# Kernel tuning notes

Hardware: AMD Instinct MI355X
Metric: run time of the kernel (lower is better)

The kernel has to match this reference:

```python
import jax, jax.numpy as jnp
import numpy as np

DIM = 1024
HEADS = 16
HEAD_DIM = DIM // HEADS
HIDDEN = DIM * 4
EPS = 1e-6


def _layernorm(x, g, b):
    mu = jnp.mean(x, axis=-1, keepdims=True)
    var = jnp.mean(jnp.square(x - mu), axis=-1, keepdims=True)
    return (x - mu) * jax.lax.rsqrt(var + EPS) * g + b


def setup_inputs() -> dict:
    key = jax.random.key(0)
    ks = jax.random.split(key, 12)
    s = 0.02
    return {
        "x": jax.random.normal(ks[0], (16, 1024, DIM), dtype=jnp.float32),
        "ln1_g": jnp.ones((DIM,), jnp.float32),
        "ln1_b": jnp.zeros((DIM,), jnp.float32),
        "qkv_w": jax.random.normal(ks[1], (DIM, 3 * DIM), jnp.float32) * s,
        "qkv_b": jnp.zeros((3 * DIM,), jnp.float32),
        "proj_w": jax.random.normal(ks[2], (DIM, DIM), jnp.float32) * s,
        "proj_b": jnp.zeros((DIM,), jnp.float32),
        "ls1_g": jnp.ones((DIM,), jnp.float32),
        "ln2_g": jnp.ones((DIM,), jnp.float32),
        "ln2_b": jnp.zeros((DIM,), jnp.float32),
        "fc1_w": jax.random.normal(ks[3], (DIM, HIDDEN), jnp.float32) * s,
        "fc1_b": jnp.zeros((HIDDEN,), jnp.float32),
        "fc2_w": jax.random.normal(ks[4], (HIDDEN, DIM), jnp.float32) * s,
        "fc2_b": jnp.zeros((DIM,), jnp.float32),
        "ls2_g": jnp.ones((DIM,), jnp.float32),
    }


def reference(x, ln1_g, ln1_b, qkv_w, qkv_b, proj_w, proj_b, ls1_g,
              ln2_g, ln2_b, fc1_w, fc1_b, fc2_w, fc2_b, ls2_g):
    B, N, C = x.shape
    # --- attention branch (NOTE: original code omits 1/sqrt(d) scaling) ---
    h = _layernorm(x, ln1_g, ln1_b)
    qkv = (h @ qkv_w + qkv_b).reshape(B, N, 3, HEADS, HEAD_DIM)
    q, k, v = jnp.moveaxis(qkv, 2, 0)          # each [B, N, H, D]
    attn = jnp.einsum("bqhd,bkhd->bhqk", q, k)  # no scale, faithful to source
    attn = jax.nn.softmax(attn, axis=-1)
    out = jnp.einsum("bhqk,bkhd->bqhd", attn, v).reshape(B, N, C)
    x = x + (out @ proj_w + proj_b) * ls1_g
    # --- MLP branch ---
    h = _layernorm(x, ln2_g, ln2_b)
    h = jax.nn.gelu(h @ fc1_w + fc1_b, approximate=False)
    x = x + (h @ fc2_w + fc2_b) * ls2_g
    return x
```

## Files before the change

kernel.cpp:

```cpp
#include <hip/hip_runtime.h>
#include <hip/hip_bf16.h>
#include <math.h>

typedef __attribute__((ext_vector_type(8))) short short8;
typedef __attribute__((ext_vector_type(4))) float f32x4;

#define MFMA16(a,b,c) __builtin_amdgcn_mfma_f32_16x16x32_bf16((a),(b),(c),0,0,0)

__device__ __forceinline__ unsigned short f2bf(float f){
  unsigned int u = __builtin_bit_cast(unsigned int, f);
  u += 0x7fffu + ((u >> 16) & 1u);
  return (unsigned short)(u >> 16);
}

__device__ __forceinline__ void gload16(const void* g, void* lds){
  __builtin_amdgcn_global_load_lds(
      (const __attribute__((address_space(1))) unsigned int*)g,
      (__attribute__((address_space(3))) unsigned int*)lds, 16, 0, 0);
}

__global__ __launch_bounds__(256) void k_transpose_cast(const float* __restrict__ in,
    unsigned short* __restrict__ out, int K, int N)
{
  __shared__ unsigned short tile[32][33];
  const int tx = threadIdx.x, ty = threadIdx.y;
  const int n0 = blockIdx.x * 32, k0 = blockIdx.y * 32;
  #pragma unroll
  for (int i = 0; i < 4; i++) {
    int k = k0 + ty + i*8;
    tile[ty + i*8][tx] = f2bf(in[(size_t)k * N + n0 + tx]);
  }
  __syncthreads();
  #pragma unroll
  for (int i = 0; i < 4; i++) {
    int n = n0 + ty + i*8;
    out[(size_t)n * K + k0 + tx] = tile[tx][ty + i*8];
  }
}

__global__ __launch_bounds__(256) void k_layernorm(const float* __restrict__ x,
    const float* __restrict__ g, const float* __restrict__ b,
    unsigned short* __restrict__ out)
{
  const int row = blockIdx.x;
  const int t = threadIdx.x;
  const float4 v = ((const float4*)(x + (size_t)row * 1024))[t];
  float s  = v.x + v.y + v.z + v.w;
  float s2 = v.x*v.x + v.y*v.y + v.z*v.z + v.w*v.w;
  #pragma unroll
  for (int m = 1; m < 64; m <<= 1) {
    s  += __shfl_xor(s,  m);
    s2 += __shfl_xor(s2, m);
  }
  __shared__ float red[2][4];
  const int wid = t >> 6, lane = t & 63;
  if (lane == 0) { red[0][wid] = s; red[1][wid] = s2; }
  __syncthreads();
  s  = red[0][0] + red[0][1] + red[0][2] + red[0][3];
  s2 = red[1][0] + red[1][1] + red[1][2] + red[1][3];
  const float mu = s * (1.0f / 1024.0f);
  const float var = s2 * (1.0f / 1024.0f) - mu * mu;
  const float rstd = rsqrtf(var + 1e-6f);
  const float4 gv = ((const float4*)g)[t];
  const float4 bv = ((const float4*)b)[t];
  ushort4 o;
  o.x = f2bf((v.x - mu) * rstd * gv.x + bv.x);
  o.y = f2bf((v.y - mu) * rstd * gv.y + bv.y);
  o.z = f2bf((v.z - mu) * rstd * gv.z + bv.z);
  o.w = f2bf((v.w - mu) * rstd * gv.w + bv.w);
  ((ushort4*)(out + (size_t)row * 1024))[t] = o;
}

template<int EPI>
__global__ __launch_bounds__(256, 3) void k_gemm128(
    const unsigned short* __restrict__ A,
    const unsigned short* __restrict__ Bt,
    const float* __restrict__ bias,
    const float* __restrict__ resid,
    const float* __restrict__ lsg,
    void* __restrict__ outp,
    unsigned short* __restrict__ vtp,
    int M, int N, int K, int nbn)
{
  __shared__ __align__(16) unsigned short Asm[128 * 32];
  __shared__ __align__(16) unsigned short Bsm[128 * 32];

  const int bid = blockIdx.x;
  const int mrows = (gridDim.x >> 3) / nbn;
  const int xcd = bid & 7, l = bid >> 3;
  const int bm = xcd * mrows + (l % mrows);
  const int bn = l / mrows;

  const int t = threadIdx.x, lane = t & 63;
  const int wid = t >> 6, wm = wid >> 1, wn = wid & 1;
  const int fr = lane & 15, fg = lane >> 4;

  const int r0 = t >> 2;
  const int c0 = ((t & 3) ^ ((r0 >> 2) & 3)) * 8;
  const int r1 = (256 + t) >> 2;
  const int c1 = (((256 + t) & 3) ^ ((r1 >> 2) & 3)) * 8;
  const size_t a0 = ((size_t)bm * 128 + r0) * K + c0;
  const size_t a1 = ((size_t)bm * 128 + r1) * K + c1;
  const size_t b0 = ((size_t)bn * 128 + r0) * K + c0;
  const size_t b1 = ((size_t)bn * 128 + r1) * K + c1;

  f32x4 acc[4][4] = {};

  for (int kt = 0; kt < K; kt += 32) {
    __syncthreads();
    gload16(A  + a0 + kt, (char*)Asm + t * 16);
    gload16(A  + a1 + kt, (char*)Asm + 4096 + t * 16);
    gload16(Bt + b0 + kt, (char*)Bsm + t * 16);
    gload16(Bt + b1 + kt, (char*)Bsm + 4096 + t * 16);
    __syncthreads();
    short8 af[4], bfv[4];
    #pragma unroll
    for (int m = 0; m < 4; m++) {
      const int row = wm * 64 + m * 16 + fr;
      af[m] = *(const short8*)((const char*)Asm + row * 64
                               + ((fg ^ ((row >> 2) & 3)) * 16));
    }
    #pragma unroll
    for (int n = 0; n < 4; n++) {
      const int row = wn * 64 + n * 16 + fr;
      bfv[n] = *(const short8*)((const char*)Bsm + row * 64
                                + ((fg ^ ((row >> 2) & 3)) * 16));
    }
    #pragma unroll
    for (int m = 0; m < 4; m++)
      #pragma unroll
      for (int n = 0; n < 4; n++)
        acc[m][n] = MFMA16(af[m], bfv[n], acc[m][n]);
  }

  const int row0 = bm * 128 + wm * 64 + fg * 4;
  const int col0 = bn * 128 + wn * 64 + fr;
  #pragma unroll
  for (int n = 0; n < 4; n++) {
    const int col = col0 + n * 16;
    const float bcol = bias[col];
    float lscale = 0.f;
    if (EPI == 2) lscale = lsg[col];
    #pragma unroll
    for (int m = 0; m < 4; m++) {
      #pragma unroll
      for (int r = 0; r < 4; r++) {
        const int row = row0 + m * 16 + r;
        float v = acc[m][n][r] + bcol;
        if (EPI == 0) {
          if (bn < 16) {
            ((unsigned short*)outp)[(size_t)row * 2048 + col] = f2bf(v);
          } else {
            const int d = col - 2048, hh = d >> 6, dd = d & 63;
            const int bb = row >> 10, nn = row & 1023;
            vtp[(((size_t)bb * 16 + hh) * 64 + dd) * 1024 + nn] = f2bf(v);
          }
        } else if (EPI == 1) {
          const float u = v * (0.7978845608f + 0.0356774081f * v * v);
          v = v * __builtin_amdgcn_rcpf(1.0f + __expf(-2.0f * u));
          ((unsigned short*)outp)[(size_t)row * N + col] = f2bf(v);
        } else {
          ((float*)outp)[(size_t)row * N + col] =
              resid[(size_t)row * N + col] + v * lscale;
        }
      }
    }
  }
}

__global__ __launch_bounds__(512) void k_attn(const unsigned short* __restrict__ qk,
                                              const unsigned short* __restrict__ vT,
                                              unsigned short* __restrict__ out)
{
  const int qt = blockIdx.x;
  const int bh = blockIdx.y;
  const int b = bh >> 4, h = bh & 15;
  const int t = threadIdx.x, lane = t & 63, wid = t >> 6;
  const int fr = lane & 15, fg = lane >> 4;
  const int q0 = qt * 256 + wid * 32;

  __shared__ __align__(16) unsigned short Ksm[64 * 64];
  __shared__ __align__(16) unsigned short Vsm[64 * 64];
  __shared__ __align__(16) unsigned short plds[8][32][72];

  const size_t qbase = (size_t)b * 1024 * 2048 + (size_t)h * 64;
  const size_t kbase = qbase + 1024;
  const size_t vbase = (size_t)bh * 64 * 1024;

  short8 qf[2][2];
  #pragma unroll
  for (int m = 0; m < 2; m++)
    #pragma unroll
    for (int kh = 0; kh < 2; kh++)
      qf[m][kh] = *(const short8*)(qk + qbase + (size_t)(q0 + m*16 + fr) * 2048
                                   + kh*32 + fg*8);

  f32x4 oacc[2][4] = {};
  float mrow[2][4], lrow[2][4];
  #pragma unroll
  for (int m = 0; m < 2; m++)
    #pragma unroll
    for (int r = 0; r < 4; r++) { mrow[m][r] = -1e30f; lrow[m][r] = 0.f; }

  const int srow = t >> 3, sc = t & 7;
  const int scs = sc ^ (srow & 7);

  for (int kv0 = 0; kv0 < 1024; kv0 += 64) {
    __syncthreads();
    gload16(qk + kbase + (size_t)(kv0 + srow) * 2048 + scs*8, (char*)Ksm + t*16);
    gload16(vT + vbase + (size_t)srow * 1024 + kv0 + scs*8,   (char*)Vsm + t*16);
    __syncthreads();

    f32x4 sacc[2][4] = {};
    #pragma unroll
    for (int n = 0; n < 4; n++) {
      #pragma unroll
      for (int kh = 0; kh < 2; kh++) {
        const int krow = n*16 + fr;
        short8 kf = *(const short8*)&Ksm[krow*64 + (((kh*4 + fg) ^ (krow & 7)) * 8)];
        sacc[0][n] = MFMA16(qf[0][kh], kf, sacc[0][n]);
        sacc[1][n] = MFMA16(qf[1][kh], kf, sacc[1][n]);
      }
    }

    #pragma unroll
    for (int m = 0; m < 2; m++) {
      float pm[4];
      #pragma unroll
      for (int r = 0; r < 4; r++)
        pm[r] = fmaxf(fmaxf(sacc[m][0][r], sacc[m][1][r]),
                      fmaxf(sacc[m][2][r], sacc[m][3][r]));
      #pragma unroll
      for (int msk = 1; msk < 16; msk <<= 1)
        #pragma unroll
        for (int r = 0; r < 4; r++) pm[r] = fmaxf(pm[r], __shfl_xor(pm[r], msk));
      float corr[4];
      #pragma unroll
      for (int r = 0; r < 4; r++) {
        float mn = fmaxf(mrow[m][r], pm[r]);
        corr[r] = __expf(mrow[m][r] - mn);
        mrow[m][r] = mn;
      }
      float psum[4] = {0.f, 0.f, 0.f, 0.f};
      #pragma unroll
      for (int n = 0; n < 4; n++)
        #pragma unroll
        for (int r = 0; r < 4; r++) {
          float p = __expf(sacc[m][n][r] - mrow[m][r]);
          sacc[m][n][r] = p;
          psum[r] += p;
        }
      #pragma unroll
      for (int msk = 1; msk < 16; msk <<= 1)
        #pragma unroll
        for (int r = 0; r < 4; r++) psum[r] += __shfl_xor(psum[r], msk);
      #pragma unroll
      for (int r = 0; r < 4; r++) lrow[m][r] = lrow[m][r] * corr[r] + psum[r];
      #pragma unroll
      for (int d16 = 0; d16 < 4; d16++)
        #pragma unroll
        for (int r = 0; r < 4; r++) oacc[m][d16][r] *= corr[r];
      #pragma unroll
      for (int n = 0; n < 4; n++)
        #pragma unroll
        for (int r = 0; r < 4; r++)
          plds[wid][m*16 + fg*4 + r][n*16 + fr] = f2bf(sacc[m][n][r]);
    }

    short8 pf[2][2];
    #pragma unroll
    for (int m = 0; m < 2; m++)
      #pragma unroll
      for (int kh = 0; kh < 2; kh++)
        pf[m][kh] = *(const short8*)&plds[wid][m*16 + fr][kh*32 + fg*8];

    #pragma unroll
    for (int d16 = 0; d16 < 4; d16++) {
      #pragma unroll
      for (int kh = 0; kh < 2; kh++) {
        const int vrow = d16*16 + fr;
        short8 vf = *(const short8*)&Vsm[vrow*64 + (((kh*4 + fg) ^ (vrow & 7)) * 8)];
        oacc[0][d16] = MFMA16(pf[0][kh], vf, oacc[0][d16]);
        oacc[1][d16] = MFMA16(pf[1][kh], vf, oacc[1][d16]);
      }
    }
  }

  #pragma unroll
  for (int m = 0; m < 2; m++) {
    float inv[4];
    #pragma unroll
    for (int r = 0; r < 4; r++) inv[r] = 1.0f / lrow[m][r];
    #pragma unroll
    for (int d16 = 0; d16 < 4; d16++) {
      #pragma unroll
      for (int r = 0; r < 4; r++) {
        const int qrow = q0 + m*16 + fg*4 + r;
        const int col = h*64 + d16*16 + fr;
        out[(size_t)(b * 1024 + qrow) * 1024 + col] = f2bf(oacc[m][d16][r] * inv[r]);
      }
    }
  }
}

extern "C" void kernel_launch(void* const* d_in, const int* in_sizes, int n_in,
                              void* d_out, int out_size, void* d_ws, size_t ws_size,
                              hipStream_t stream) {
  const float* x      = (const float*)d_in[0];
  const float* ln1_g  = (const float*)d_in[1];
  const float* ln1_b  = (const float*)d_in[2];
  const float* qkv_w  = (const float*)d_in[3];
  const float* qkv_b  = (const float*)d_in[4];
  const float* proj_w = (const float*)d_in[5];
  const float* proj_b = (const float*)d_in[6];
  const float* ls1_g  = (const float*)d_in[7];
  const float* ln2_g  = (const float*)d_in[8];
  const float* ln2_b  = (const float*)d_in[9];
  const float* fc1_w  = (const float*)d_in[10];
  const float* fc1_b  = (const float*)d_in[11];
  const float* fc2_w  = (const float*)d_in[12];
  const float* fc2_b  = (const float*)d_in[13];
  const float* ls2_g  = (const float*)d_in[14];

  char* w = (char*)d_ws;
  unsigned short* wqkvT  = (unsigned short*)(w + 0);
  unsigned short* wprojT = (unsigned short*)(w + 6291456);
  unsigned short* wfc1T  = (unsigned short*)(w + 8388608);
  unsigned short* wfc2T  = (unsigned short*)(w + 16777216);
  float*          x1     = (float*)(w + 25165824);
  unsigned short* h1     = (unsigned short*)(w + 92274688);
  unsigned short* qkbuf  = (unsigned short*)(w + 125829120);
  unsigned short* vtbuf  = (unsigned short*)(w + 192937984);
  unsigned short* attno  = (unsigned short*)(w + 226492416);
  unsigned short* h3     = (unsigned short*)(w + 125829120);

  dim3 tb32(32, 8);
  k_transpose_cast<<<dim3(3072/32, 1024/32), tb32, 0, stream>>>(qkv_w,  wqkvT, 1024, 3072);
  k_transpose_cast<<<dim3(1024/32, 1024/32), tb32, 0, stream>>>(proj_w, wprojT, 1024, 1024);
  k_transpose_cast<<<dim3(4096/32, 1024/32), tb32, 0, stream>>>(fc1_w,  wfc1T, 1024, 4096);
  k_transpose_cast<<<dim3(1024/32, 4096/32), tb32, 0, stream>>>(fc2_w,  wfc2T, 4096, 1024);

  k_layernorm<<<16384, 256, 0, stream>>>(x, ln1_g, ln1_b, h1);
  k_gemm128<0><<<128*24, 256, 0, stream>>>(h1, wqkvT, qkv_b, nullptr, nullptr,
                                           qkbuf, vtbuf, 16384, 3072, 1024, 24);
  k_attn<<<dim3(4, 256), 512, 0, stream>>>(qkbuf, vtbuf, attno);
  k_gemm128<2><<<128*8, 256, 0, stream>>>(attno, wprojT, proj_b, x, ls1_g,
                                          x1, nullptr, 16384, 1024, 1024, 8);
  k_layernorm<<<16384, 256, 0, stream>>>(x1, ln2_g, ln2_b, h1);
  k_gemm128<1><<<128*32, 256, 0, stream>>>(h1, wfc1T, fc1_b, nullptr, nullptr,
                                           h3, nullptr, 16384, 4096, 1024, 32);
  k_gemm128<2><<<128*8, 256, 0, stream>>>(h3, wfc2T, fc2_b, x1, ls2_g,
                                          (float*)d_out, nullptr, 16384, 1024, 4096, 8);
}
```

Measured before the change: 854.4 us.

## Double GEMM K-tile to 64, store residual x1 in bf16, add MFMA priority

```diff
diff --git a/kernel.cpp b/kernel.cpp
--- a/kernel.cpp
+++ b/kernel.cpp
@@ -11,6 +11,10 @@
   unsigned int u = __builtin_bit_cast(unsigned int, f);
   u += 0x7fffu + ((u >> 16) & 1u);
   return (unsigned short)(u >> 16);
+}
+__device__ __forceinline__ float bf2f(unsigned short u){
+  unsigned int v = ((unsigned int)u) << 16;
+  return __builtin_bit_cast(float, v);
 }
 
 __device__ __forceinline__ void gload16(const void* g, void* lds){
@@ -38,13 +42,20 @@
   }
 }
 
-__global__ __launch_bounds__(256) void k_layernorm(const float* __restrict__ x,
+template<int BF16IN>
+__global__ __launch_bounds__(256) void k_layernorm(const void* __restrict__ xin,
     const float* __restrict__ g, const float* __restrict__ b,
     unsigned short* __restrict__ out)
 {
   const int row = blockIdx.x;
   const int t = threadIdx.x;
-  const float4 v = ((const float4*)(x + (size_t)row * 1024))[t];
+  float4 v;
+  if (BF16IN) {
+    const ushort4 u = ((const ushort4*)((const unsigned short*)xin + (size_t)row * 1024))[t];
+    v.x = bf2f(u.x); v.y = bf2f(u.y); v.z = bf2f(u.z); v.w = bf2f(u.w);
+  } else {
+    v = ((const float4*)((const float*)xin + (size_t)row * 1024))[t];
+  }
   float s  = v.x + v.y + v.z + v.w;
   float s2 = v.x*v.x + v.y*v.y + v.z*v.z + v.w*v.w;
   #pragma unroll
@@ -76,14 +87,14 @@
     const unsigned short* __restrict__ A,
     const unsigned short* __restrict__ Bt,
     const float* __restrict__ bias,
-    const float* __restrict__ resid,
+    const void* __restrict__ resid,
     const float* __restrict__ lsg,
     void* __restrict__ outp,
     unsigned short* __restrict__ vtp,
     int M, int N, int K, int nbn)
 {
-  __shared__ __align__(16) unsigned short Asm[128 * 32];
-  __shared__ __align__(16) unsigned short Bsm[128 * 32];
+  __shared__ __align__(16) unsigned short Asm[128 * 64];
+  __shared__ __align__(16) unsigned short Bsm[128 * 64];
 
   const int bid = blockIdx.x;
   const int mrows = (gridDim.x >> 3) / nbn;
@@ -95,42 +106,52 @@
   const int wid = t >> 6, wm = wid >> 1, wn = wid & 1;
   const int fr = lane & 15, fg = lane >> 4;
 
-  const int r0 = t >> 2;
-  const int c0 = ((t & 3) ^ ((r0 >> 2) & 3)) * 8;
-  const int r1 = (256 + t) >> 2;
-  const int c1 = (((256 + t) & 3) ^ ((r1 >> 2) & 3)) * 8;
-  const size_t a0 = ((size_t)bm * 128 + r0) * K + c0;
-  const size_t a1 = ((size_t)bm * 128 + r1) * K + c1;
-  const size_t b0 = ((size_t)bn * 128 + r0) * K + c0;
-  const size_t b1 = ((size_t)bn * 128 + r1) * K + c1;
+  size_t aOf[4], bOf[4];
+  int dOf[4];
+  #pragma unroll
+  for (int i = 0; i < 4; i++) {
+    const int s = i * 256 + t;
+    const int row = s >> 3, c = s & 7;
+    const int cs = c ^ (row & 7);
+    dOf[i] = s * 16;
+    aOf[i] = ((size_t)bm * 128 + row) * K + cs * 8;
+    bOf[i] = ((size_t)bn * 128 + row) * K + cs * 8;
+  }
 
   f32x4 acc[4][4] = {};
 
-  for (int kt = 0; kt < K; kt += 32) {
+  for (int kt = 0; kt < K; kt += 64) {
     __syncthreads();
-    gload16(A  + a0 + kt, (char*)Asm + t * 16);
-    gload16(A  + a1 + kt, (char*)Asm + 4096 + t * 16);
-    gload16(Bt + b0 + kt, (char*)Bsm + t * 16);
-    gload16(Bt + b1 + kt, (char*)Bsm + 4096 + t * 16);
+    #pragma unroll
+    for (int i = 0; i < 4; i++) gload16(A  + aOf[i] + kt, (char*)Asm + dOf[i]);
+    #pragma unroll
+    for (int i = 0; i < 4; i++) gload16(Bt + bOf[i] + kt, (char*)Bsm + dOf[i]);
     __syncthreads();
-    short8 af[4], bfv[4];
+
+    short8 af[4][2], bfv[4][2];
     #pragma unroll
     for (int m = 0; m < 4; m++) {
       const int row = wm * 64 + m * 16 + fr;
-      af[m] = *(const short8*)((const char*)Asm + row * 64
-                               + ((fg ^ ((row >> 2) & 3)) * 16));
+      const char* p = (const char*)Asm + row * 128;
+      af[m][0] = *(const short8*)(p + ((fg       ^ (row & 7)) * 16));
+      af[m][1] = *(const short8*)(p + (((4 + fg) ^ (row & 7)) * 16));
     }
     #pragma unroll
     for (int n = 0; n < 4; n++) {
       const int row = wn * 64 + n * 16 + fr;
-      bfv[n] = *(const short8*)((const char*)Bsm + row * 64
-                                + ((fg ^ ((row >> 2) & 3)) * 16));
-    }
-    #pragma unroll
-    for (int m = 0; m < 4; m++)
-      #pragma unroll
-      for (int n = 0; n < 4; n++)
-        acc[m][n] = MFMA16(af[m], bfv[n], acc[m][n]);
+      const char* p = (const char*)Bsm + row * 128;
+      bfv[n][0] = *(const short8*)(p + ((fg       ^ (row & 7)) * 16));
+      bfv[n][1] = *(const short8*)(p + (((4 + fg) ^ (row & 7)) * 16));
+    }
+    __builtin_amdgcn_s_setprio(1);
+    #pragma unroll
+    for (int kk = 0; kk < 2; kk++)
+      #pragma unroll
+      for (int m = 0; m < 4; m++)
+        #pragma unroll
+        for (int n = 0; n < 4; n++)
+          acc[m][n] = MFMA16(af[m][kk], bfv[n][kk], acc[m][n]);
+    __builtin_amdgcn_s_setprio(0);
   }
 
   const int row0 = bm * 128 + wm * 64 + fg * 4;
@@ -140,7 +161,7 @@
     const int col = col0 + n * 16;
     const float bcol = bias[col];
     float lscale = 0.f;
-    if (EPI == 2) lscale = lsg[col];
+    if (EPI >= 2) lscale = lsg[col];
     #pragma unroll
     for (int m = 0; m < 4; m++) {
       #pragma unroll
@@ -159,9 +180,12 @@
           const float u = v * (0.7978845608f + 0.0356774081f * v * v);
           v = v * __builtin_amdgcn_rcpf(1.0f + __expf(-2.0f * u));
           ((unsigned short*)outp)[(size_t)row * N + col] = f2bf(v);
+        } else if (EPI == 2) {
+          const float rv = ((const float*)resid)[(size_t)row * N + col];
+          ((unsigned short*)outp)[(size_t)row * N + col] = f2bf(rv + v * lscale);
         } else {
-          ((float*)outp)[(size_t)row * N + col] =
-              resid[(size_t)row * N + col] + v * lscale;
+          const float rv = bf2f(((const unsigned short*)resid)[(size_t)row * N + col]);
+          ((float*)outp)[(size_t)row * N + col] = rv + v * lscale;
         }
       }
     }
@@ -327,12 +351,12 @@
   unsigned short* wprojT = (unsigned short*)(w + 6291456);
   unsigned short* wfc1T  = (unsigned short*)(w + 8388608);
   unsigned short* wfc2T  = (unsigned short*)(w + 16777216);
-  float*          x1     = (float*)(w + 25165824);
-  unsigned short* h1     = (unsigned short*)(w + 92274688);
-  unsigned short* qkbuf  = (unsigned short*)(w + 125829120);
-  unsigned short* vtbuf  = (unsigned short*)(w + 192937984);
-  unsigned short* attno  = (unsigned short*)(w + 226492416);
-  unsigned short* h3     = (unsigned short*)(w + 125829120);
+  unsigned short* x1     = (unsigned short*)(w + 25165824);
+  unsigned short* h1     = (unsigned short*)(w + 58720256);
+  unsigned short* qkbuf  = (unsigned short*)(w + 92274688);
+  unsigned short* vtbuf  = (unsigned short*)(w + 159383552);
+  unsigned short* attno  = (unsigned short*)(w + 192937984);
+  unsigned short* h3     = (unsigned short*)(w + 92274688);
 
   dim3 tb32(32, 8);
   k_transpose_cast<<<dim3(3072/32, 1024/32), tb32, 0, stream>>>(qkv_w,  wqkvT, 1024, 3072);
@@ -340,15 +364,15 @@
   k_transpose_cast<<<dim3(4096/32, 1024/32), tb32, 0, stream>>>(fc1_w,  wfc1T, 1024, 4096);
   k_transpose_cast<<<dim3(1024/32, 4096/32), tb32, 0, stream>>>(fc2_w,  wfc2T, 4096, 1024);
 
-  k_layernorm<<<16384, 256, 0, stream>>>(x, ln1_g, ln1_b, h1);
+  k_layernorm<0><<<16384, 256, 0, stream>>>(x, ln1_g, ln1_b, h1);
   k_gemm128<0><<<128*24, 256, 0, stream>>>(h1, wqkvT, qkv_b, nullptr, nullptr,
                                            qkbuf, vtbuf, 16384, 3072, 1024, 24);
   k_attn<<<dim3(4, 256), 512, 0, stream>>>(qkbuf, vtbuf, attno);
   k_gemm128<2><<<128*8, 256, 0, stream>>>(attno, wprojT, proj_b, x, ls1_g,
                                           x1, nullptr, 16384, 1024, 1024, 8);
-  k_layernorm<<<16384, 256, 0, stream>>>(x1, ln2_g, ln2_b, h1);
+  k_layernorm<1><<<16384, 256, 0, stream>>>(x1, ln2_g, ln2_b, h1);
   k_gemm128<1><<<128*32, 256, 0, stream>>>(h1, wfc1T, fc1_b, nullptr, nullptr,
                                            h3, nullptr, 16384, 4096, 1024, 32);
-  k_gemm128<2><<<128*8, 256, 0, stream>>>(h3, wfc2T, fc2_b, x1, ls2_g,
+  k_gemm128<3><<<128*8, 256, 0, stream>>>(h3, wfc2T, fc2_b, x1, ls2_g,
                                           (float*)d_out, nullptr, 16384, 1024, 4096, 8);
 }
```

After: 795.6 us. -6.9%, faster.
